# Kernel optimization log

Measured on AMD Instinct MI355X. Metric: run time of the kernel, lower is better.

## Reference

```python
import jax, jax.numpy as jnp
import numpy as np

B, N, D_MODEL, H = 4, 2048, 1024, 16  # batch, seq, model dim, heads


def setup_inputs() -> dict:
    key = jax.random.key(0)
    k1, k2, k3 = jax.random.split(key, 3)
    x = jax.random.normal(k1, (B, N, D_MODEL), dtype=jnp.float32)
    # nn.Linear weights: [out_features, in_features]; scaled for stability
    Wqkv = jax.random.normal(k2, (3 * D_MODEL, D_MODEL), dtype=jnp.float32) * 0.02
    bqkv = jnp.zeros((3 * D_MODEL,), dtype=jnp.float32)
    Wo = jax.random.normal(k3, (D_MODEL, D_MODEL), dtype=jnp.float32) * 0.02
    bo = jnp.zeros((D_MODEL,), dtype=jnp.float32)
    return {"x": x, "Wqkv": Wqkv, "bqkv": bqkv, "Wo": Wo, "bo": bo}


def reference(x, Wqkv, bqkv, Wo, bo):
    b, n, _ = x.shape
    qkv = x @ Wqkv.T + bqkv                      # [b, n, 3*d_model]
    # rearrange 'b n (h d) -> b h n d' with h heads, then chunk into q,k,v
    qkv = qkv.reshape(b, n, H, -1).transpose(0, 2, 1, 3)  # [b, h, n, 3*dh]
    q, k, v = jnp.split(qkv, 3, axis=-1)          # each [b, h, n, dh]
    scale = k.shape[-1] ** 0.5
    scores = jnp.einsum('bhqd,bhkd->bhqk', q, k) / scale
    attn = jax.nn.softmax(scores, axis=-1)
    out = jnp.einsum('bhqk,bhkd->bhqd', attn, v)  # [b, h, n, dh]
    out = out.transpose(0, 2, 1, 3).reshape(b, n, -1)  # 'b h n d -> b n (h d)'
    return out @ Wo.T + bo
```

## Files before the change

### kernel.cpp

```cpp
#include <hip/hip_runtime.h>
#include <hip/hip_bf16.h>

using bf16 = __hip_bfloat16;
typedef __attribute__((ext_vector_type(8))) __bf16 bf16x8;
typedef __attribute__((ext_vector_type(4))) float f32x4;
typedef __attribute__((ext_vector_type(16))) float f32x16;
typedef __attribute__((ext_vector_type(4))) unsigned u32x4;

#define MFMA16(a, b, c) __builtin_amdgcn_mfma_f32_16x16x32_bf16((a), (b), (c), 0, 0, 0)
#define MFMA32(a, b, c) __builtin_amdgcn_mfma_f32_32x32x16_bf16((a), (b), (c), 0, 0, 0)

#define WAITV4 asm volatile("s_waitcnt vmcnt(4)" ::: "memory")
#define WAITV2 asm volatile("s_waitcnt vmcnt(2)" ::: "memory")
#define WAITV0 asm volatile("s_waitcnt vmcnt(0)" ::: "memory")
#define WAITL0 asm volatile("s_waitcnt lgkmcnt(0)" ::: "memory")
#define BAR    __builtin_amdgcn_s_barrier()
#define SCHED0 __builtin_amdgcn_sched_barrier(0)

static __device__ __forceinline__ void gload_lds16(const bf16* g, bf16* l) {
    __builtin_amdgcn_global_load_lds(
        (__attribute__((address_space(1))) void*)(bf16*)(g),
        (__attribute__((address_space(3))) void*)(l), 16, 0, 0);
}

static __device__ __forceinline__ unsigned cvtpk(float lo, float hi) {
    unsigned r;
    asm("v_cvt_pk_bf16_f32 %0, %1, %2" : "=v"(r) : "v"(lo), "v"(hi));
    return r;
}

__global__ void cvt_all(const float* __restrict__ x, const float* __restrict__ wq,
                        const float* __restrict__ wo,
                        bf16* __restrict__ xb, bf16* __restrict__ wqb, bf16* __restrict__ wob) {
    int b = blockIdx.x;
    const float* src;
    bf16* dst;
    long i;
    if (b < 8192)       { src = x;  dst = xb;  i = (long)b * 256 + threadIdx.x; }
    else if (b < 11264) { src = wq; dst = wqb; i = (long)(b - 8192) * 256 + threadIdx.x; }
    else                { src = wo; dst = wob; i = (long)(b - 11264) * 256 + threadIdx.x; }
    float4 v = ((const float4*)src)[i];
    bf16 t[4];
    t[0] = __float2bfloat16(v.x);
    t[1] = __float2bfloat16(v.y);
    t[2] = __float2bfloat16(v.z);
    t[3] = __float2bfloat16(v.w);
    *(uint2*)(dst + 4l * i) = *(uint2*)t;
}


#define GEMM_STAGE(AB, BB, K0)                                             \
    do {                                                                   \
        gload_lds16(Ab + (long)srow * K + (K0) + scol, (AB) + t * 8);      \
        gload_lds16(Ab + (long)(srow + 64) * K + (K0) + scol, (AB) + 2048 + t * 8); \
        gload_lds16(Bb + (long)srow * K + (K0) + scol, (BB) + t * 8);      \
        gload_lds16(Bb + (long)(srow + 64) * K + (K0) + scol, (BB) + 2048 + t * 8); \
    } while (0)

#define GEMM_COMPUTE(AB, BB)                                               \
    do {                                                                   \
        bf16x8 af[4], bfv[4];                                              \
        _Pragma("unroll") for (int mi4 = 0; mi4 < 4; mi4++)                \
            af[mi4] = *(const bf16x8*)((AB) + (wm * 64 + mi4 * 16 + r) * 32 + q * 8); \
        _Pragma("unroll") for (int ni4 = 0; ni4 < 4; ni4++)                \
            bfv[ni4] = *(const bf16x8*)((BB) + (wn * 64 + ni4 * 16 + r) * 32 + q * 8); \
        __builtin_amdgcn_s_setprio(1);                                     \
        _Pragma("unroll") for (int mi4 = 0; mi4 < 4; mi4++)                \
            _Pragma("unroll") for (int ni4 = 0; ni4 < 4; ni4++)            \
                acc[mi4][ni4] = MFMA16(af[mi4], bfv[ni4], acc[mi4][ni4]);  \
        __builtin_amdgcn_s_setprio(0);                                     \
    } while (0)

#define GEMM_MAIN_LOOP                                                     \
    GEMM_STAGE(A0, B0, 0);                                                 \
    GEMM_STAGE(A1, B1, 32);                                                \
    for (int k0 = 0; k0 < K - 64; k0 += 64) {                              \
        WAITV4; BAR; SCHED0;                                               \
        GEMM_COMPUTE(A0, B0);                                              \
        WAITL0; BAR; SCHED0;                                               \
        GEMM_STAGE(A0, B0, k0 + 64);                                       \
        WAITV4; BAR; SCHED0;                                               \
        GEMM_COMPUTE(A1, B1);                                              \
        WAITL0; BAR; SCHED0;                                               \
        if (k0 + 96 < K) GEMM_STAGE(A1, B1, k0 + 96);                      \
    }                                                                      \
    WAITV4; BAR; SCHED0;                                                   \
    GEMM_COMPUTE(A0, B0);                                                  \
    WAITV0; BAR; SCHED0;                                                   \
    GEMM_COMPUTE(A1, B1);

__global__ void gemm_qkv(const bf16* __restrict__ A, const bf16* __restrict__ B,
                         const float* __restrict__ bias,
                         bf16* __restrict__ Qo, bf16* __restrict__ Ko, bf16* __restrict__ Vt) {
    const int K = 1024;
    __shared__ bf16 smem[16384];
    bf16* A0 = smem;
    bf16* B0 = smem + 4096;
    bf16* A1 = smem + 8192;
    bf16* B1 = smem + 12288;
    int t = threadIdx.x;
    int lane = t & 63;
    int wave = t >> 6;
    int wm = wave >> 1, wn = wave & 1;
    int r = lane & 15, q = lane >> 4;
    int lin = blockIdx.x;
    int xcd = lin & 7, rr_ = lin >> 3;
    int mi = xcd * 8 + rr_ / 24;
    int ni = rr_ % 24;
    long m0 = (long)mi * 128;
    long n0 = (long)ni * 128;
    const bf16* Ab = A + m0 * K;
    const bf16* Bb = B + n0 * K;

    f32x4 acc[4][4] = {};

    int srow = t >> 2;
    int scol = (t & 3) << 3;

    GEMM_MAIN_LOOP

#pragma unroll
    for (int ni4 = 0; ni4 < 4; ni4++) {
        int n = (int)n0 + wn * 64 + ni4 * 16 + r;
        float bn = bias[n];
        int h = n / 192;
        int rem = n % 192;
        int part = rem >> 6;
        int d = rem & 63;
#pragma unroll
        for (int mi4 = 0; mi4 < 4; mi4++) {
#pragma unroll
            for (int rr = 0; rr < 4; rr++) {
                int m = (int)m0 + wm * 64 + mi4 * 16 + q * 4 + rr;
                int b = m >> 11;
                int row = m & 2047;
                long bh = b * 16 + h;
                bf16 bv = __float2bfloat16(acc[mi4][ni4][rr] + bn);
                if (part == 0)      Qo[(bh * 2048 + row) * 64 + d] = bv;
                else if (part == 1) Ko[(bh * 2048 + row) * 64 + d] = bv;
                else                Vt[(bh * 64 + d) * 2048 + row] = bv;
            }
        }
    }
}


#define PACK8(S, OFF, OUTV) { \
    unsigned A0_ = cvtpk(S[OFF+0], S[OFF+1]); \
    unsigned B0_ = cvtpk(S[OFF+4], S[OFF+5]); \
    unsigned A1_ = cvtpk(S[OFF+2], S[OFF+3]); \
    unsigned B1_ = cvtpk(S[OFF+6], S[OFF+7]); \
    asm("v_permlane32_swap_b32 %0, %1" : "+v"(A0_), "+v"(B0_)); \
    asm("v_permlane32_swap_b32 %0, %1" : "+v"(A1_), "+v"(B1_)); \
    u32x4 W; W.x = A0_; W.y = A1_; W.z = B0_; W.w = B1_; \
    OUTV = __builtin_bit_cast(bf16x8, W); }

#define COMPUTE(KB, VB) do { \
    f32x16 sA = {}, sB = {}; \
    __builtin_amdgcn_s_setprio(1); \
    { \
        bf16x8 kA, kB; \
        kA = *(const bf16x8*)(KB + (0 * 64 + lane) * 8); \
        kB = *(const bf16x8*)(KB + (256 + 0 * 64 + lane) * 8); \
        sA = MFMA32(kA, qf0, sA);  sB = MFMA32(kB, qf0, sB); \
        kA = *(const bf16x8*)(KB + (1 * 64 + lane) * 8); \
        kB = *(const bf16x8*)(KB + (256 + 1 * 64 + lane) * 8); \
        sA = MFMA32(kA, qf1, sA);  sB = MFMA32(kB, qf1, sB); \
        kA = *(const bf16x8*)(KB + (2 * 64 + lane) * 8); \
        kB = *(const bf16x8*)(KB + (256 + 2 * 64 + lane) * 8); \
        sA = MFMA32(kA, qf2, sA);  sB = MFMA32(kB, qf2, sB); \
        kA = *(const bf16x8*)(KB + (3 * 64 + lane) * 8); \
        kB = *(const bf16x8*)(KB + (256 + 3 * 64 + lane) * 8); \
        sA = MFMA32(kA, qf3, sA);  sB = MFMA32(kB, qf3, sB); \
    } \
    __builtin_amdgcn_s_setprio(0); \
    float x0 = fmaxf(fmaxf(sA[0], sA[1]), fmaxf(sA[2], sA[3])); \
    float x1 = fmaxf(fmaxf(sA[4], sA[5]), fmaxf(sA[6], sA[7])); \
    float x2 = fmaxf(fmaxf(sA[8], sA[9]), fmaxf(sA[10], sA[11])); \
    float x3 = fmaxf(fmaxf(sA[12], sA[13]), fmaxf(sA[14], sA[15])); \
    float y0 = fmaxf(fmaxf(sB[0], sB[1]), fmaxf(sB[2], sB[3])); \
    float y1 = fmaxf(fmaxf(sB[4], sB[5]), fmaxf(sB[6], sB[7])); \
    float y2 = fmaxf(fmaxf(sB[8], sB[9]), fmaxf(sB[10], sB[11])); \
    float y3 = fmaxf(fmaxf(sB[12], sB[13]), fmaxf(sB[14], sB[15])); \
    float pm = fmaxf(fmaxf(fmaxf(x0, x1), fmaxf(x2, x3)), \
                     fmaxf(fmaxf(y0, y1), fmaxf(y2, y3))); \
    pm = fmaxf(pm, __shfl_xor(pm, 32)); \
    bool resc = !__all(pm <= mv + 8.0f); \
    if (resc) { \
        float mn = fmaxf(mv, pm); \
        float al = __builtin_amdgcn_exp2f((mv - mn) * C1); \
        mv = mn; \
        lv *= al; \
        _Pragma("unroll") for (int e = 0; e < 16; ++e) { o0[e] *= al; o1[e] *= al; } \
    } \
    float mc = mv * C1; \
    _Pragma("unroll") for (int e = 0; e < 16; ++e) sA[e] = __builtin_amdgcn_exp2f(sA[e] * C1 - mc); \
    _Pragma("unroll") for (int e = 0; e < 16; ++e) sB[e] = __builtin_amdgcn_exp2f(sB[e] * C1 - mc); \
    { \
        f32x16 scv = sA + sB; \
        float u0 = (scv[0] + scv[1]) + (scv[2] + scv[3]); \
        float u1 = (scv[4] + scv[5]) + (scv[6] + scv[7]); \
        float u2 = (scv[8] + scv[9]) + (scv[10] + scv[11]); \
        float u3 = (scv[12] + scv[13]) + (scv[14] + scv[15]); \
        float ts = (u0 + u1) + (u2 + u3); \
        ts += __shfl_xor(ts, 32); \
        lv += ts; \
    } \
    bf16x8 pf0, pf1, pf2, pf3; \
    PACK8(sA, 0, pf0); PACK8(sA, 8, pf1); PACK8(sB, 0, pf2); PACK8(sB, 8, pf3); \
    __builtin_amdgcn_s_setprio(1); \
    { \
        bf16x8 vA, vB; \
        vA = *(const bf16x8*)(VB + (0 * 64 + lane) * 8); \
        vB = *(const bf16x8*)(VB + (256 + 0 * 64 + lane) * 8); \
        o0 = MFMA32(vA, pf0, o0);  o1 = MFMA32(vB, pf0, o1); \
        vA = *(const bf16x8*)(VB + (1 * 64 + lane) * 8); \
        vB = *(const bf16x8*)(VB + (256 + 1 * 64 + lane) * 8); \
        o0 = MFMA32(vA, pf1, o0);  o1 = MFMA32(vB, pf1, o1); \
        vA = *(const bf16x8*)(VB + (2 * 64 + lane) * 8); \
        vB = *(const bf16x8*)(VB + (256 + 2 * 64 + lane) * 8); \
        o0 = MFMA32(vA, pf2, o0);  o1 = MFMA32(vB, pf2, o1); \
        vA = *(const bf16x8*)(VB + (3 * 64 + lane) * 8); \
        vB = *(const bf16x8*)(VB + (256 + 3 * 64 + lane) * 8); \
        o0 = MFMA32(vA, pf3, o0);  o1 = MFMA32(vB, pf3, o1); \
    } \
    __builtin_amdgcn_s_setprio(0); \
} while (0)

__global__ __launch_bounds__(512, 4) void attn_fwd(const bf16* __restrict__ Q,
                                                   const bf16* __restrict__ Kg,
                                                   const bf16* __restrict__ Vt,
                                                   bf16* __restrict__ AO) {
    __shared__ bf16 smem[16384];
    bf16* K0 = smem;
    bf16* V0 = smem + 4096;
    bf16* K1 = smem + 8192;
    bf16* V1 = smem + 12288;
    const int t = threadIdx.x;
    const int lane = t & 63, wave = t >> 6;
    const int l31 = lane & 31, hi = lane >> 5;
    const int bid = blockIdx.x;
    const int xcd = bid & 7, idx = bid >> 3;
    const int bh = xcd * 8 + (idx >> 3);
    const int qt = idx & 7;
    const float C1 = 0.18033688011112042f;

    bf16x8 qf0, qf1, qf2, qf3;
    {
        const bf16* Qb = Q + ((long)bh * 2048 + qt * 256 + wave * 32 + l31) * 64 + hi * 8;
        qf0 = *(const bf16x8*)(Qb + 0);
        qf1 = *(const bf16x8*)(Qb + 16);
        qf2 = *(const bf16x8*)(Qb + 32);
        qf3 = *(const bf16x8*)(Qb + 48);
    }

    const bf16* Kh = Kg + (long)bh * 2048 * 64;
    const bf16* Vh = Vt + (long)bh * 64 * 2048;

    const int sr = ((t >> 8) << 5) + (t & 31);
    const int sc = ((t >> 6) & 3) * 16 + ((t >> 5) & 1) * 8;

    f32x16 o0 = {}, o1 = {};
    float mv = -1e30f, lv = 0.f;

    auto issue_stage = [&](bf16* Kb, bf16* Vb, int kv0) {
        gload_lds16(Kh + (long)(kv0 + sr) * 64 + sc, Kb + t * 8);
        gload_lds16(Vh + (long)sr * 2048 + kv0 + sc, Vb + t * 8);
    };

    issue_stage(K0, V0, 0);
    issue_stage(K1, V1, 64);

    for (int kv0 = 0; kv0 < 2048 - 128; kv0 += 128) {
        WAITV2; BAR; SCHED0;
        COMPUTE(K0, V0);
        WAITL0; BAR; SCHED0;
        issue_stage(K0, V0, kv0 + 128);
        WAITV2; BAR; SCHED0;
        COMPUTE(K1, V1);
        WAITL0; BAR; SCHED0;
        if (kv0 + 192 < 2048) issue_stage(K1, V1, kv0 + 192);
    }
    WAITV2; BAR; SCHED0;
    COMPUTE(K0, V0);
    WAITV0; BAR; SCHED0;
    COMPUTE(K1, V1);

    long bb = bh >> 4, hh = bh & 15;
    __syncthreads();
    float il = 1.f / lv;
    char* wbase = (char*)smem + wave * 4096 + l31 * 128;
#pragma unroll
    for (int j = 0; j < 4; ++j) {
        unsigned wlo = cvtpk(o0[4 * j] * il, o0[4 * j + 1] * il);
        unsigned whi = cvtpk(o0[4 * j + 2] * il, o0[4 * j + 3] * il);
        int b8 = 2 * j + hi;
        int b8s = b8 ^ ((l31 & 7) << 1);
        uint2 val; val.x = wlo; val.y = whi;
        *(uint2*)(wbase + b8s * 8) = val;
    }
#pragma unroll
    for (int j = 0; j < 4; ++j) {
        unsigned wlo = cvtpk(o1[4 * j] * il, o1[4 * j + 1] * il);
        unsigned whi = cvtpk(o1[4 * j + 2] * il, o1[4 * j + 3] * il);
        int b8 = 8 + 2 * j + hi;
        int b8s = b8 ^ ((l31 & 7) << 1);
        uint2 val; val.x = wlo; val.y = whi;
        *(uint2*)(wbase + b8s * 8) = val;
    }
    __syncthreads();
    {
        int rid = t >> 1, hf = t & 1;
        int wv = rid >> 5, qq = rid & 31;
        long orow = (long)qt * 256 + wv * 32 + qq;
        const char* rbase = (const char*)smem + wv * 4096 + qq * 128;
        bf16* dst = AO + (bb * 2048 + orow) * 1024 + hh * 64 + hf * 32;
#pragma unroll
        for (int k = 0; k < 4; ++k) {
            int b8 = hf * 8 + 2 * k;
            int b8s = b8 ^ ((qq & 7) << 1);
            int4 v = *(const int4*)(rbase + b8s * 8);
            *(int4*)(dst + k * 8) = v;
        }
    }
}

__global__ void gemm_out(const bf16* __restrict__ A, const bf16* __restrict__ B,
                         const float* __restrict__ bias, float* __restrict__ C) {
    const int K = 1024, N = 1024;
    __shared__ bf16 smem[16384];
    bf16* A0 = smem;
    bf16* B0 = smem + 4096;
    bf16* A1 = smem + 8192;
    bf16* B1 = smem + 12288;
    int t = threadIdx.x;
    int lane = t & 63;
    int wave = t >> 6;
    int wm = wave >> 1, wn = wave & 1;
    int r = lane & 15, q = lane >> 4;
    int lin = blockIdx.x;
    int xcd = lin & 7, rr_ = lin >> 3;
    int mi = xcd * 8 + (rr_ >> 3);
    int ni = rr_ & 7;
    long m0 = (long)mi * 128;
    long n0 = (long)ni * 128;
    const bf16* Ab = A + m0 * K;
    const bf16* Bb = B + n0 * K;

    f32x4 acc[4][4] = {};

    int srow = t >> 2;
    int scol = (t & 3) << 3;

    GEMM_MAIN_LOOP

#pragma unroll
    for (int ni4 = 0; ni4 < 4; ni4++) {
        int n = (int)n0 + wn * 64 + ni4 * 16 + r;
        float bn = bias[n];
#pragma unroll
        for (int mi4 = 0; mi4 < 4; mi4++) {
#pragma unroll
            for (int rr = 0; rr < 4; rr++) {
                long m = m0 + wm * 64 + mi4 * 16 + q * 4 + rr;
                C[m * N + n] = acc[mi4][ni4][rr] + bn;
            }
        }
    }
}

extern "C" void kernel_launch(void* const* d_in, const int* in_sizes, int n_in,
                              void* d_out, int out_size, void* d_ws, size_t ws_size,
                              hipStream_t stream) {
    const float* x    = (const float*)d_in[0];
    const float* Wqkv = (const float*)d_in[1];
    const float* bqkv = (const float*)d_in[2];
    const float* Wo   = (const float*)d_in[3];
    const float* bo   = (const float*)d_in[4];
    float* out = (float*)d_out;

    char* ws = (char*)d_ws;
    bf16* Xb  = (bf16*)(ws + 0);
    bf16* Wqb = (bf16*)(ws + 16777216);
    bf16* Wob = (bf16*)(ws + 23068672);
    bf16* Qb  = (bf16*)(ws + 25165824);
    bf16* Kb  = (bf16*)(ws + 41943040);
    bf16* Vtb = (bf16*)(ws + 58720256);
    bf16* AOb = (bf16*)(ws + 75497472);

    cvt_all<<<12288, 256, 0, stream>>>(x, Wqkv, Wo, Xb, Wqb, Wob);

    gemm_qkv<<<1536, 256, 0, stream>>>(Xb, Wqb, bqkv, Qb, Kb, Vtb);
    attn_fwd<<<512, 512, 0, stream>>>(Qb, Kb, Vtb, AOb);
    gemm_out<<<512, 256, 0, stream>>>(AOb, Wob, bo, out);
}
```

Before: 202.0 us.

## Use 32x32 MFMA in QKV GEMM and restructure attention KV pipeline

```diff
diff --git a/kernel.cpp b/kernel.cpp
--- a/kernel.cpp
+++ b/kernel.cpp
@@ -11,7 +11,6 @@
 #define MFMA32(a, b, c) __builtin_amdgcn_mfma_f32_32x32x16_bf16((a), (b), (c), 0, 0, 0)
 
 #define WAITV4 asm volatile("s_waitcnt vmcnt(4)" ::: "memory")
-#define WAITV2 asm volatile("s_waitcnt vmcnt(2)" ::: "memory")
 #define WAITV0 asm volatile("s_waitcnt vmcnt(0)" ::: "memory")
 #define WAITL0 asm volatile("s_waitcnt lgkmcnt(0)" ::: "memory")
 #define BAR    __builtin_amdgcn_s_barrier()
@@ -49,45 +48,52 @@
 }
 
 
-#define GEMM_STAGE(AB, BB, K0)                                             \
-    do {                                                                   \
-        gload_lds16(Ab + (long)srow * K + (K0) + scol, (AB) + t * 8);      \
-        gload_lds16(Ab + (long)(srow + 64) * K + (K0) + scol, (AB) + 2048 + t * 8); \
-        gload_lds16(Bb + (long)srow * K + (K0) + scol, (BB) + t * 8);      \
-        gload_lds16(Bb + (long)(srow + 64) * K + (K0) + scol, (BB) + 2048 + t * 8); \
-    } while (0)
-
-#define GEMM_COMPUTE(AB, BB)                                               \
-    do {                                                                   \
-        bf16x8 af[4], bfv[4];                                              \
-        _Pragma("unroll") for (int mi4 = 0; mi4 < 4; mi4++)                \
-            af[mi4] = *(const bf16x8*)((AB) + (wm * 64 + mi4 * 16 + r) * 32 + q * 8); \
-        _Pragma("unroll") for (int ni4 = 0; ni4 < 4; ni4++)                \
-            bfv[ni4] = *(const bf16x8*)((BB) + (wn * 64 + ni4 * 16 + r) * 32 + q * 8); \
-        __builtin_amdgcn_s_setprio(1);                                     \
-        _Pragma("unroll") for (int mi4 = 0; mi4 < 4; mi4++)                \
-            _Pragma("unroll") for (int ni4 = 0; ni4 < 4; ni4++)            \
-                acc[mi4][ni4] = MFMA16(af[mi4], bfv[ni4], acc[mi4][ni4]);  \
-        __builtin_amdgcn_s_setprio(0);                                     \
-    } while (0)
-
-#define GEMM_MAIN_LOOP                                                     \
-    GEMM_STAGE(A0, B0, 0);                                                 \
-    GEMM_STAGE(A1, B1, 32);                                                \
-    for (int k0 = 0; k0 < K - 64; k0 += 64) {                              \
-        WAITV4; BAR; SCHED0;                                               \
-        GEMM_COMPUTE(A0, B0);                                              \
-        WAITL0; BAR; SCHED0;                                               \
-        GEMM_STAGE(A0, B0, k0 + 64);                                       \
-        WAITV4; BAR; SCHED0;                                               \
-        GEMM_COMPUTE(A1, B1);                                              \
-        WAITL0; BAR; SCHED0;                                               \
-        if (k0 + 96 < K) GEMM_STAGE(A1, B1, k0 + 96);                      \
-    }                                                                      \
-    WAITV4; BAR; SCHED0;                                                   \
-    GEMM_COMPUTE(A0, B0);                                                  \
-    WAITV0; BAR; SCHED0;                                                   \
-    GEMM_COMPUTE(A1, B1);
+#define G32_STAGE(AB, BB, K0) do { \
+    gload_lds16(Ab + (long)(wave * 32 + l31) * K + (K0) + hi * 8,      (AB) + t * 8); \
+    gload_lds16(Ab + (long)(wave * 32 + l31) * K + (K0) + 16 + hi * 8, (AB) + (256 + t) * 8); \
+    gload_lds16(Bb + (long)(wave * 32 + l31) * K + (K0) + hi * 8,      (BB) + t * 8); \
+    gload_lds16(Bb + (long)(wave * 32 + l31) * K + (K0) + 16 + hi * 8, (BB) + (256 + t) * 8); \
+} while (0)
+
+#define G32_COMPUTE(AB, BB) do { \
+    bf16x8 aA0 = *(const bf16x8*)((AB) + ((wm2)*64 + lane) * 8); \
+    bf16x8 aB0 = *(const bf16x8*)((AB) + ((wm2 + 1)*64 + lane) * 8); \
+    bf16x8 aA1 = *(const bf16x8*)((AB) + (256 + (wm2)*64 + lane) * 8); \
+    bf16x8 aB1 = *(const bf16x8*)((AB) + (256 + (wm2 + 1)*64 + lane) * 8); \
+    bf16x8 bA0 = *(const bf16x8*)((BB) + ((wn2)*64 + lane) * 8); \
+    bf16x8 bB0 = *(const bf16x8*)((BB) + ((wn2 + 1)*64 + lane) * 8); \
+    bf16x8 bA1 = *(const bf16x8*)((BB) + (256 + (wn2)*64 + lane) * 8); \
+    bf16x8 bB1 = *(const bf16x8*)((BB) + (256 + (wn2 + 1)*64 + lane) * 8); \
+    __builtin_amdgcn_s_setprio(1); \
+    acc00 = MFMA32(aA0, bA0, acc00); \
+    acc01 = MFMA32(aA0, bB0, acc01); \
+    acc10 = MFMA32(aB0, bA0, acc10); \
+    acc11 = MFMA32(aB0, bB0, acc11); \
+    acc00 = MFMA32(aA1, bA1, acc00); \
+    acc01 = MFMA32(aA1, bB1, acc01); \
+    acc10 = MFMA32(aB1, bA1, acc10); \
+    acc11 = MFMA32(aB1, bB1, acc11); \
+    __builtin_amdgcn_s_setprio(0); \
+} while (0)
+
+#define G32_EPI(ACC, MB, NB) do { \
+    int n = (int)n0 + wn * 64 + (NB) * 32 + l31; \
+    float bn = bias[n]; \
+    int h = n / 192; \
+    int rem = n % 192; \
+    int part = rem >> 6; \
+    int d = rem & 63; \
+    _Pragma("unroll") for (int g = 0; g < 16; ++g) { \
+        int m = (int)m0 + wm * 64 + (MB) * 32 + (g & 3) + 8 * (g >> 2) + 4 * hi; \
+        int b = m >> 11; \
+        int row = m & 2047; \
+        long bh = b * 16 + h; \
+        bf16 bv = __float2bfloat16(ACC[g] + bn); \
+        if (part == 0)      Qo[(bh * 2048 + row) * 64 + d] = bv; \
+        else if (part == 1) Ko[(bh * 2048 + row) * 64 + d] = bv; \
+        else                Vt[(bh * 64 + d) * 2048 + row] = bv; \
+    } \
+} while (0)
 
 __global__ void gemm_qkv(const bf16* __restrict__ A, const bf16* __restrict__ B,
                          const float* __restrict__ bias,
@@ -102,7 +108,8 @@
     int lane = t & 63;
     int wave = t >> 6;
     int wm = wave >> 1, wn = wave & 1;
-    int r = lane & 15, q = lane >> 4;
+    int wm2 = wm * 2, wn2 = wn * 2;
+    int l31 = lane & 31, hi = lane >> 5;
     int lin = blockIdx.x;
     int xcd = lin & 7, rr_ = lin >> 3;
     int mi = xcd * 8 + rr_ / 24;
@@ -112,36 +119,29 @@
     const bf16* Ab = A + m0 * K;
     const bf16* Bb = B + n0 * K;
 
-    f32x4 acc[4][4] = {};
-
-    int srow = t >> 2;
-    int scol = (t & 3) << 3;
-
-    GEMM_MAIN_LOOP
-
-#pragma unroll
-    for (int ni4 = 0; ni4 < 4; ni4++) {
-        int n = (int)n0 + wn * 64 + ni4 * 16 + r;
-        float bn = bias[n];
-        int h = n / 192;
-        int rem = n % 192;
-        int part = rem >> 6;
-        int d = rem & 63;
-#pragma unroll
-        for (int mi4 = 0; mi4 < 4; mi4++) {
-#pragma unroll
-            for (int rr = 0; rr < 4; rr++) {
-                int m = (int)m0 + wm * 64 + mi4 * 16 + q * 4 + rr;
-                int b = m >> 11;
-                int row = m & 2047;
-                long bh = b * 16 + h;
-                bf16 bv = __float2bfloat16(acc[mi4][ni4][rr] + bn);
-                if (part == 0)      Qo[(bh * 2048 + row) * 64 + d] = bv;
-                else if (part == 1) Ko[(bh * 2048 + row) * 64 + d] = bv;
-                else                Vt[(bh * 64 + d) * 2048 + row] = bv;
-            }
-        }
-    }
+    f32x16 acc00 = {}, acc01 = {}, acc10 = {}, acc11 = {};
+
+    G32_STAGE(A0, B0, 0);
+    G32_STAGE(A1, B1, 32);
+    for (int k0 = 0; k0 < K - 64; k0 += 64) {
+        WAITV4; BAR; SCHED0;
+        G32_COMPUTE(A0, B0);
+        WAITL0; BAR; SCHED0;
+        G32_STAGE(A0, B0, k0 + 64);
+        WAITV4; BAR; SCHED0;
+        G32_COMPUTE(A1, B1);
+        WAITL0; BAR; SCHED0;
+        if (k0 + 96 < K) G32_STAGE(A1, B1, k0 + 96);
+    }
+    WAITV4; BAR; SCHED0;
+    G32_COMPUTE(A0, B0);
+    WAITV0; BAR; SCHED0;
+    G32_COMPUTE(A1, B1);
+
+    G32_EPI(acc00, 0, 0);
+    G32_EPI(acc01, 0, 1);
+    G32_EPI(acc10, 1, 0);
+    G32_EPI(acc11, 1, 1);
 }
 
 
@@ -194,18 +194,11 @@
         _Pragma("unroll") for (int e = 0; e < 16; ++e) { o0[e] *= al; o1[e] *= al; } \
     } \
     float mc = mv * C1; \
-    _Pragma("unroll") for (int e = 0; e < 16; ++e) sA[e] = __builtin_amdgcn_exp2f(sA[e] * C1 - mc); \
-    _Pragma("unroll") for (int e = 0; e < 16; ++e) sB[e] = __builtin_amdgcn_exp2f(sB[e] * C1 - mc); \
-    { \
-        f32x16 scv = sA + sB; \
-        float u0 = (scv[0] + scv[1]) + (scv[2] + scv[3]); \
-        float u1 = (scv[4] + scv[5]) + (scv[6] + scv[7]); \
-        float u2 = (scv[8] + scv[9]) + (scv[10] + scv[11]); \
-        float u3 = (scv[12] + scv[13]) + (scv[14] + scv[15]); \
-        float ts = (u0 + u1) + (u2 + u3); \
-        ts += __shfl_xor(ts, 32); \
-        lv += ts; \
-    } \
+    float ts = 0.f; \
+    _Pragma("unroll") for (int e = 0; e < 16; ++e) { float p = __builtin_amdgcn_exp2f(sA[e] * C1 - mc); sA[e] = p; ts += p; } \
+    _Pragma("unroll") for (int e = 0; e < 16; ++e) { float p = __builtin_amdgcn_exp2f(sB[e] * C1 - mc); sB[e] = p; ts += p; } \
+    ts += __shfl_xor(ts, 32); \
+    lv += ts; \
     bf16x8 pf0, pf1, pf2, pf3; \
     PACK8(sA, 0, pf0); PACK8(sA, 8, pf1); PACK8(sB, 0, pf2); PACK8(sB, 8, pf3); \
     __builtin_amdgcn_s_setprio(1); \
@@ -269,22 +262,17 @@
     };
 
     issue_stage(K0, V0, 0);
-    issue_stage(K1, V1, 64);
-
-    for (int kv0 = 0; kv0 < 2048 - 128; kv0 += 128) {
-        WAITV2; BAR; SCHED0;
+    __syncthreads();
+
+    for (int kv0 = 0;; kv0 += 128) {
+        issue_stage(K1, V1, kv0 + 64);
         COMPUTE(K0, V0);
-        WAITL0; BAR; SCHED0;
-        issue_stage(K0, V0, kv0 + 128);
-        WAITV2; BAR; SCHED0;
+        __syncthreads();
+        if (kv0 + 128 < 2048) issue_stage(K0, V0, kv0 + 128);
         COMPUTE(K1, V1);
-        WAITL0; BAR; SCHED0;
-        if (kv0 + 192 < 2048) issue_stage(K1, V1, kv0 + 192);
-    }
-    WAITV2; BAR; SCHED0;
-    COMPUTE(K0, V0);
-    WAITV0; BAR; SCHED0;
-    COMPUTE(K1, V1);
+        if (kv0 + 128 >= 2048) break;
+        __syncthreads();
+    }
 
     long bb = bh >> 4, hh = bh & 15;
     __syncthreads();
@@ -324,6 +312,28 @@
         }
     }
 }
+
+#define GEMM_STAGE(AB, BB, K0)                                             \
+    do {                                                                   \
+        gload_lds16(Ab + (long)srow * K + (K0) + scol, (AB) + t * 8);      \
+        gload_lds16(Ab + (long)(srow + 64) * K + (K0) + scol, (AB) + 2048 + t * 8); \
+        gload_lds16(Bb + (long)srow * K + (K0) + scol, (BB) + t * 8);      \
+        gload_lds16(Bb + (long)(srow + 64) * K + (K0) + scol, (BB) + 2048 + t * 8); \
+    } while (0)
+
+#define GEMM_COMPUTE(AB, BB)                                               \
+    do {                                                                   \
+        bf16x8 af[4], bfv[4];                                              \
+        _Pragma("unroll") for (int mi4 = 0; mi4 < 4; mi4++)                \
+            af[mi4] = *(const bf16x8*)((AB) + (wm * 64 + mi4 * 16 + r) * 32 + q * 8); \
+        _Pragma("unroll") for (int ni4 = 0; ni4 < 4; ni4++)                \
+            bfv[ni4] = *(const bf16x8*)((BB) + (wn * 64 + ni4 * 16 + r) * 32 + q * 8); \
+        __builtin_amdgcn_s_setprio(1);                                     \
+        _Pragma("unroll") for (int mi4 = 0; mi4 < 4; mi4++)                \
+            _Pragma("unroll") for (int ni4 = 0; ni4 < 4; ni4++)            \
+                acc[mi4][ni4] = MFMA16(af[mi4], bfv[ni4], acc[mi4][ni4]);  \
+        __builtin_amdgcn_s_setprio(0);                                     \
+    } while (0)
 
 __global__ void gemm_out(const bf16* __restrict__ A, const bf16* __restrict__ B,
                          const float* __restrict__ bias, float* __restrict__ C) {
@@ -352,7 +362,22 @@
     int srow = t >> 2;
     int scol = (t & 3) << 3;
 
-    GEMM_MAIN_LOOP
+    GEMM_STAGE(A0, B0, 0);
+    GEMM_STAGE(A1, B1, 32);
+    for (int k0 = 0; k0 < K - 64; k0 += 64) {
+        WAITV4; BAR; SCHED0;
+        GEMM_COMPUTE(A0, B0);
+        WAITL0; BAR; SCHED0;
+        GEMM_STAGE(A0, B0, k0 + 64);
+        WAITV4; BAR; SCHED0;
+        GEMM_COMPUTE(A1, B1);
+        WAITL0; BAR; SCHED0;
+        if (k0 + 96 < K) GEMM_STAGE(A1, B1, k0 + 96);
+    }
+    WAITV4; BAR; SCHED0;
+    GEMM_COMPUTE(A0, B0);
+    WAITV0; BAR; SCHED0;
+    GEMM_COMPUTE(A1, B1);
 
 #pragma unroll
     for (int ni4 = 0; ni4 < 4; ni4++) {
```

After: 246.6 us. 22.1% more time.
